# Optimization experiments

Hardware: AMD Instinct MI355X
Metric: run time of the kernel (lower is better)

The kernel has to match this reference:

```python
import jax, jax.numpy as jnp
import numpy as np

B, S, D = 4, 4096, 64

def setup_inputs() -> dict:
    key = jax.random.key(0)
    k1, k2 = jax.random.split(key)
    query = jax.random.normal(k1, (B, S, D), dtype=jnp.float32)
    value = jax.random.normal(k2, (B, S, D), dtype=jnp.float32)
    return {"query": query, "value": value}

def reference(query, value):
    # score = Q @ V^T  -> [B, Sq, Skv]  (note: value acts as both key and value; no 1/sqrt(d) scaling)
    score = jnp.einsum("bqd,bkd->bqk", query, value)
    attn_weights = jax.nn.softmax(score, axis=-1)
    context = jnp.einsum("bqk,bkd->bqd", attn_weights, value)
    return (context, attn_weights)
```

## Files before the change

kernel.cpp:

```cpp
#include <hip/hip_runtime.h>

#define BB 4
#define SS 4096
#define DD 64
#define QB 32
#define TK 64
#define SV 72
#define SP 72

typedef _Float16 h16;
typedef h16 half4_t __attribute__((ext_vector_type(4)));
typedef h16 half8_t __attribute__((ext_vector_type(8)));
typedef float f32x4 __attribute__((ext_vector_type(4)));

struct LdsBufs {
    h16 Vhi[2][TK * SV];
    h16 Vlo[2][TK * SV];
    h16 VTr[2][DD * SV];
    h16 Pl[4][16 * SP];
};

__device__ __forceinline__ void stage(LdsBufs& L, const float* Vb, int it, int t,
                                      bool with_vt) {
    const int ts  = t >> 7;
    const int tt  = t & 127;
    const int c16 = tt & 15;
    const int kr  = tt >> 4;
    const f32x4* Vg = (const f32x4*)(Vb + ((size_t)(it * 2 + ts) * TK + kr * 8) * DD);
    half4_t hh[8];
#pragma unroll
    for (int i = 0; i < 8; ++i) {
        f32x4 v = Vg[i * 16 + c16];
        half4_t hi, lo;
#pragma unroll
        for (int j = 0; j < 4; ++j) {
            float x = v[j];
            h16 h = (h16)x;
            hi[j] = h;
            lo[j] = (h16)(x - (float)h);
        }
        hh[i] = hi;
        *(half4_t*)&L.Vhi[ts][(kr * 8 + i) * SV + c16 * 4] = hi;
        *(half4_t*)&L.Vlo[ts][(kr * 8 + i) * SV + c16 * 4] = lo;
    }
    if (with_vt) {
#pragma unroll
        for (int j = 0; j < 4; ++j) {
            half8_t col;
#pragma unroll
            for (int i = 0; i < 8; ++i) col[i] = hh[i][j];
            *(half8_t*)&L.VTr[ts][(c16 * 4 + j) * SV + kr * 8] = col;
        }
    }
}

__device__ __forceinline__ void scores(const LdsBufs& L, int ts, int qi, int quad,
                                       const half8_t* qhi, const half8_t* qlo,
                                       f32x4* sc) {
#pragma unroll
    for (int mt = 0; mt < 4; ++mt) sc[mt] = (f32x4){0.f, 0.f, 0.f, 0.f};
#pragma unroll
    for (int ks = 0; ks < 2; ++ks) {
#pragma unroll
        for (int mt = 0; mt < 4; ++mt) {
            half8_t ahi = *(const half8_t*)&L.Vhi[ts][(mt * 16 + qi) * SV + ks * 32 + quad * 8];
            half8_t alo = *(const half8_t*)&L.Vlo[ts][(mt * 16 + qi) * SV + ks * 32 + quad * 8];
            sc[mt] = __builtin_amdgcn_mfma_f32_16x16x32_f16(ahi, qhi[ks], sc[mt], 0, 0, 0);
            sc[mt] = __builtin_amdgcn_mfma_f32_16x16x32_f16(ahi, qlo[ks], sc[mt], 0, 0, 0);
            sc[mt] = __builtin_amdgcn_mfma_f32_16x16x32_f16(alo, qhi[ks], sc[mt], 0, 0, 0);
        }
    }
}

__global__ __launch_bounds__(256, 2) void attn_fused(const float* __restrict__ Q,
                                                     const float* __restrict__ V,
                                                     float* __restrict__ ctx,
                                                     float* __restrict__ attn) {
    __shared__ LdsBufs L;
    const int t     = threadIdx.x;
    const int w     = t >> 6;
    const int lane  = t & 63;
    const int qi    = lane & 15;
    const int quad  = lane >> 4;
    const int qgrp  = w & 1;
    const int khalf = w >> 1;
    const int b     = blockIdx.y;
    const int qb    = blockIdx.x * QB + qgrp * 16;

    const float* Vb   = V + (size_t)b * SS * DD;
    const float* Qrow = Q + ((size_t)b * SS + qb + qi) * DD;

    half8_t qhi[2], qlo[2];
#pragma unroll
    for (int ks = 0; ks < 2; ++ks) {
        const float* p = Qrow + ks * 32 + quad * 8;
#pragma unroll
        for (int j = 0; j < 8; ++j) {
            float x = p[j];
            h16 h = (h16)x;
            qhi[ks][j] = h;
            qlo[ks][j] = (h16)(x - (float)h);
        }
    }

    float mrun = -1e30f, lrun = 0.f;
    f32x4 oc[4];
#pragma unroll
    for (int mt = 0; mt < 4; ++mt) oc[mt] = (f32x4){0.f, 0.f, 0.f, 0.f};

    for (int it = 0; it < SS / TK / 2; ++it) {
        __syncthreads();
        stage(L, Vb, it, t, true);
        __syncthreads();

        f32x4 sc[4];
        scores(L, khalf, qi, quad, qhi, qlo, sc);

        float tmax = -1e30f;
#pragma unroll
        for (int mt = 0; mt < 4; ++mt)
#pragma unroll
            for (int r = 0; r < 4; ++r) tmax = fmaxf(tmax, sc[mt][r]);
        tmax = fmaxf(tmax, __shfl_xor(tmax, 16));
        tmax = fmaxf(tmax, __shfl_xor(tmax, 32));
        float mn    = fmaxf(mrun, tmax);
        float alpha = __expf(mrun - mn);
        float psum  = 0.f;
        half4_t pv[4];
#pragma unroll
        for (int mt = 0; mt < 4; ++mt)
#pragma unroll
            for (int r = 0; r < 4; ++r) {
                float p = __expf(sc[mt][r] - mn);
                psum += p;
                pv[mt][r] = (h16)p;
            }
        psum += __shfl_xor(psum, 16);
        psum += __shfl_xor(psum, 32);
        lrun = lrun * alpha + psum;
        mrun = mn;
#pragma unroll
        for (int mt = 0; mt < 4; ++mt) {
            oc[mt] *= alpha;
            *(half4_t*)&L.Pl[w][qi * SP + mt * 16 + quad * 4] = pv[mt];
        }

#pragma unroll
        for (int ks = 0; ks < 2; ++ks) {
            half8_t bp = *(const half8_t*)&L.Pl[w][qi * SP + ks * 32 + quad * 8];
#pragma unroll
            for (int mt = 0; mt < 4; ++mt) {
                half8_t av = *(const half8_t*)&L.VTr[khalf][(mt * 16 + qi) * SV + ks * 32 + quad * 8];
                oc[mt] = __builtin_amdgcn_mfma_f32_16x16x32_f16(av, bp, oc[mt], 0, 0, 0);
            }
        }
    }

    __syncthreads();
    {
        float* buf  = (float*)&L.Vhi[0][0];
        float* mine = buf + (w * 64 + lane) * 18;
        mine[0] = mrun;
        mine[1] = lrun;
#pragma unroll
        for (int mt = 0; mt < 4; ++mt)
#pragma unroll
            for (int r = 0; r < 4; ++r) mine[2 + mt * 4 + r] = oc[mt][r];
        __syncthreads();
        const float* po = buf + ((w ^ 2) * 64 + lane) * 18;
        float m2 = po[0], l2 = po[1];
        float mn = fmaxf(mrun, m2);
        float ea = __expf(mrun - mn), eb = __expf(m2 - mn);
        lrun = lrun * ea + l2 * eb;
#pragma unroll
        for (int mt = 0; mt < 4; ++mt)
#pragma unroll
            for (int r = 0; r < 4; ++r)
                oc[mt][r] = oc[mt][r] * ea + po[2 + mt * 4 + r] * eb;
        mrun = mn;
    }

    const float invl = 1.f / lrun;

    if (khalf == 0) {
        float* crow = ctx + ((size_t)b * SS + qb + qi) * DD;
#pragma unroll
        for (int mt = 0; mt < 4; ++mt) {
            f32x4 cv;
#pragma unroll
            for (int r = 0; r < 4; ++r) cv[r] = oc[mt][r] * invl;
            *(f32x4*)&crow[mt * 16 + quad * 4] = cv;
        }
    }

    float* arow = attn + ((size_t)b * SS + qb + qi) * SS;
    for (int it = 0; it < SS / TK / 2; ++it) {
        __syncthreads();
        stage(L, Vb, it, t, false);
        __syncthreads();

        f32x4 sc[4];
        scores(L, khalf, qi, quad, qhi, qlo, sc);
        const int kt = it * 2 + khalf;
#pragma unroll
        for (int mt = 0; mt < 4; ++mt) {
            f32x4 wv;
#pragma unroll
            for (int r = 0; r < 4; ++r) wv[r] = __expf(sc[mt][r] - mrun) * invl;
            *(f32x4*)&arow[kt * TK + mt * 16 + quad * 4] = wv;
        }
    }
}

extern "C" void kernel_launch(void* const* d_in, const int* in_sizes, int n_in,
                              void* d_out, int out_size, void* d_ws, size_t ws_size,
                              hipStream_t stream) {
    const float* Q = (const float*)d_in[0];
    const float* V = (const float*)d_in[1];
    float* ctx  = (float*)d_out;
    float* attn = (float*)d_out + (size_t)BB * SS * DD;
    attn_fused<<<dim3(SS / QB, BB), 256, 0, stream>>>(Q, V, ctx, attn);
}
```

Before: 385.3 us.

## Precompute split-fp16 V images and stream them via async global-to-LDS loads

```diff
diff --git a/kernel.cpp b/kernel.cpp
--- a/kernel.cpp
+++ b/kernel.cpp
@@ -3,212 +3,280 @@
 #define BB 4
 #define SS 4096
 #define DD 64
-#define QB 32
-#define TK 64
-#define SV 72
-#define SP 72
+#define QB 64
+#define NKI 128
+#define NIT (SS / NKI)
+#define IMGB 49152
 
 typedef _Float16 h16;
-typedef h16 half4_t __attribute__((ext_vector_type(4)));
+typedef h16 half2_t __attribute__((ext_vector_type(2)));
 typedef h16 half8_t __attribute__((ext_vector_type(8)));
 typedef float f32x4 __attribute__((ext_vector_type(4)));
-
-struct LdsBufs {
-    h16 Vhi[2][TK * SV];
-    h16 Vlo[2][TK * SV];
-    h16 VTr[2][DD * SV];
-    h16 Pl[4][16 * SP];
-};
-
-__device__ __forceinline__ void stage(LdsBufs& L, const float* Vb, int it, int t,
-                                      bool with_vt) {
-    const int ts  = t >> 7;
-    const int tt  = t & 127;
-    const int c16 = tt & 15;
-    const int kr  = tt >> 4;
-    const f32x4* Vg = (const f32x4*)(Vb + ((size_t)(it * 2 + ts) * TK + kr * 8) * DD);
-    half4_t hh[8];
-#pragma unroll
-    for (int i = 0; i < 8; ++i) {
-        f32x4 v = Vg[i * 16 + c16];
-        half4_t hi, lo;
+typedef float f32x16 __attribute__((ext_vector_type(16)));
+typedef unsigned u32x4v __attribute__((ext_vector_type(4)));
+
+typedef __attribute__((address_space(3))) uint32_t lds_u32;
+typedef const __attribute__((address_space(1))) uint32_t gl_u32;
+
+#define Z16 ((f32x16){0.f,0.f,0.f,0.f,0.f,0.f,0.f,0.f,0.f,0.f,0.f,0.f,0.f,0.f,0.f,0.f})
+
+template <int NC>
+__device__ __forceinline__ void stage_img(const char* g, char* l, int t) {
+#pragma unroll
+    for (int i = 0; i < NC; ++i) {
+        const int off = (i * 512 + t) * 16;
+        __builtin_amdgcn_global_load_lds((gl_u32*)(g + off), (lds_u32*)(l + off), 16, 0, 0);
+    }
+}
+
+__device__ __forceinline__ unsigned pkh(float a, float b) {
+    half2_t x = {(h16)a, (h16)b};
+    return __builtin_bit_cast(unsigned, x);
+}
+
+__device__ __forceinline__ void xpair(unsigned& wl, unsigned& wh, int h) {
+    unsigned xl = (unsigned)__shfl_xor((int)wl, 32);
+    unsigned xh = (unsigned)__shfl_xor((int)wh, 32);
+    unsigned nl = h ? xh : wl;
+    unsigned nh = h ? wh : xl;
+    wl = nl; wh = nh;
+}
+
+__global__ __launch_bounds__(512) void prep_v(const float* __restrict__ V,
+                                              char* __restrict__ W) {
+    __shared__ h16 VT[64][128];
+    const int t  = threadIdx.x;
+    const int it = blockIdx.x;
+    const int b  = blockIdx.y;
+    const int k  = t >> 2;
+    const int dc = t & 3;
+    char* img = W + ((size_t)b * NIT + it) * IMGB;
+    const float* src = V + ((size_t)b * SS + (size_t)it * NKI + k) * DD + dc * 16;
+#pragma unroll
+    for (int o = 0; o < 2; ++o) {
+        f32x4 a = *(const f32x4*)(src + o * 8);
+        f32x4 c = *(const f32x4*)(src + o * 8 + 4);
+        half8_t hi, lo;
 #pragma unroll
         for (int j = 0; j < 4; ++j) {
-            float x = v[j];
-            h16 h = (h16)x;
-            hi[j] = h;
-            lo[j] = (h16)(x - (float)h);
-        }
-        hh[i] = hi;
-        *(half4_t*)&L.Vhi[ts][(kr * 8 + i) * SV + c16 * 4] = hi;
-        *(half4_t*)&L.Vlo[ts][(kr * 8 + i) * SV + c16 * 4] = lo;
-    }
-    if (with_vt) {
-#pragma unroll
-        for (int j = 0; j < 4; ++j) {
-            half8_t col;
-#pragma unroll
-            for (int i = 0; i < 8; ++i) col[i] = hh[i][j];
-            *(half8_t*)&L.VTr[ts][(c16 * 4 + j) * SV + kr * 8] = col;
-        }
-    }
-}
-
-__device__ __forceinline__ void scores(const LdsBufs& L, int ts, int qi, int quad,
-                                       const half8_t* qhi, const half8_t* qlo,
-                                       f32x4* sc) {
-#pragma unroll
-    for (int mt = 0; mt < 4; ++mt) sc[mt] = (f32x4){0.f, 0.f, 0.f, 0.f};
+            float x = a[j]; h16 hh = (h16)x;
+            hi[j] = hh; lo[j] = (h16)(x - (float)hh);
+            float y = c[j]; h16 gg = (h16)y;
+            hi[j + 4] = gg; lo[j + 4] = (h16)(y - (float)gg);
+        }
+        const int cc = (dc * 2 + o) ^ (k & 7);
+        *(half8_t*)(img + (size_t)k * 128 + cc * 16) = hi;
+        *(half8_t*)(img + 16384 + (size_t)k * 128 + cc * 16) = lo;
+        const int d0 = dc * 16 + o * 8;
+#pragma unroll
+        for (int j = 0; j < 8; ++j) VT[d0 + j][k] = hi[j];
+    }
+    __syncthreads();
+#pragma unroll
+    for (int j = 0; j < 2; ++j) {
+        const int ci = j * 512 + t;
+        const int d  = ci >> 4;
+        const int cc = ci & 15;
+        const int k0 = (cc ^ (d & 7)) * 8;
+        half8_t v = *(const half8_t*)&VT[d][k0];
+        *(half8_t*)(img + 32768 + (size_t)d * 256 + cc * 16) = v;
+    }
+}
+
+__device__ __forceinline__ f32x16 scores32(const char* buf, int kq, int h, int kr, int x7,
+                                           const half8_t* qh, const half8_t* ql) {
+    const char* Vh = buf + (size_t)(kq * 32 + kr) * 128;
+    const char* Vl = Vh + 16384;
+    f32x16 sa = Z16, sb = Z16;
+#pragma unroll
+    for (int s = 0; s < 4; ++s) {
+        const int cc = ((s * 2 + h) ^ x7) << 4;
+        half8_t ah = *(const half8_t*)(Vh + cc);
+        half8_t al = *(const half8_t*)(Vl + cc);
+        if (s & 1) {
+            sb = __builtin_amdgcn_mfma_f32_32x32x16_f16(ah, qh[s], sb, 0, 0, 0);
+            sb = __builtin_amdgcn_mfma_f32_32x32x16_f16(ah, ql[s], sb, 0, 0, 0);
+            sb = __builtin_amdgcn_mfma_f32_32x32x16_f16(al, qh[s], sb, 0, 0, 0);
+        } else {
+            sa = __builtin_amdgcn_mfma_f32_32x32x16_f16(ah, qh[s], sa, 0, 0, 0);
+            sa = __builtin_amdgcn_mfma_f32_32x32x16_f16(ah, ql[s], sa, 0, 0, 0);
+            sa = __builtin_amdgcn_mfma_f32_32x32x16_f16(al, qh[s], sa, 0, 0, 0);
+        }
+    }
+    return sa + sb;
+}
+
+__device__ __forceinline__ void p1_step(const char* buf, int kq, int h, int kr, int x7,
+                                        const half8_t* qh, const half8_t* ql,
+                                        float& mrun, float& lrun, f32x16& oc0, f32x16& oc1) {
+    f32x16 sc = scores32(buf, kq, h, kr, x7, qh, ql);
+
+    float tmax = sc[0];
+#pragma unroll
+    for (int i = 1; i < 16; ++i) tmax = fmaxf(tmax, sc[i]);
+    tmax = fmaxf(tmax, __shfl_xor(tmax, 32));
+    const float mn = fmaxf(mrun, tmax);
+    float p[16], ps = 0.f;
+#pragma unroll
+    for (int i = 0; i < 16; ++i) { p[i] = __expf(sc[i] - mn); ps += p[i]; }
+    ps += __shfl_xor(ps, 32);
+    const bool still = __all(tmax <= mrun);
+    const float alpha = still ? 1.f : __expf(mrun - mn);
+    lrun = lrun * alpha + ps;
+    mrun = mn;
+    if (!still) { oc0 *= alpha; oc1 *= alpha; }
+
+    unsigned w0 = pkh(p[0], p[1]),   w1 = pkh(p[2], p[3]);
+    unsigned w2 = pkh(p[4], p[5]),   w3 = pkh(p[6], p[7]);
+    unsigned w4 = pkh(p[8], p[9]),   w5 = pkh(p[10], p[11]);
+    unsigned w6 = pkh(p[12], p[13]), w7 = pkh(p[14], p[15]);
+    xpair(w0, w2, h); xpair(w1, w3, h); xpair(w4, w6, h); xpair(w5, w7, h);
+    half8_t pb0 = __builtin_bit_cast(half8_t, (u32x4v){w0, w1, w2, w3});
+    half8_t pb1 = __builtin_bit_cast(half8_t, (u32x4v){w4, w5, w6, w7});
+
+    const char* VT = buf + 32768 + (size_t)kr * 256;
 #pragma unroll
     for (int ks = 0; ks < 2; ++ks) {
-#pragma unroll
-        for (int mt = 0; mt < 4; ++mt) {
-            half8_t ahi = *(const half8_t*)&L.Vhi[ts][(mt * 16 + qi) * SV + ks * 32 + quad * 8];
-            half8_t alo = *(const half8_t*)&L.Vlo[ts][(mt * 16 + qi) * SV + ks * 32 + quad * 8];
-            sc[mt] = __builtin_amdgcn_mfma_f32_16x16x32_f16(ahi, qhi[ks], sc[mt], 0, 0, 0);
-            sc[mt] = __builtin_amdgcn_mfma_f32_16x16x32_f16(ahi, qlo[ks], sc[mt], 0, 0, 0);
-            sc[mt] = __builtin_amdgcn_mfma_f32_16x16x32_f16(alo, qhi[ks], sc[mt], 0, 0, 0);
-        }
-    }
-}
-
-__global__ __launch_bounds__(256, 2) void attn_fused(const float* __restrict__ Q,
-                                                     const float* __restrict__ V,
+        const half8_t bp = ks ? pb1 : pb0;
+        const int c0 = ((kq * 4 + ks * 2 + h) ^ x7) << 4;
+        half8_t av0 = *(const half8_t*)(VT + c0);
+        half8_t av1 = *(const half8_t*)(VT + 32 * 256 + c0);
+        oc0 = __builtin_amdgcn_mfma_f32_32x32x16_f16(av0, bp, oc0, 0, 0, 0);
+        oc1 = __builtin_amdgcn_mfma_f32_32x32x16_f16(av1, bp, oc1, 0, 0, 0);
+    }
+}
+
+__device__ __forceinline__ void p2_step(const char* buf, int it, int kq, int h, int kr, int x7,
+                                        const half8_t* qh, const half8_t* ql,
+                                        float moff, float* arow) {
+    f32x16 sc = scores32(buf, kq, h, kr, x7, qh, ql);
+    const int colb = it * NKI + kq * 32 + h * 4;
+#pragma unroll
+    for (int g = 0; g < 4; ++g) {
+        f32x4 wv;
+#pragma unroll
+        for (int m = 0; m < 4; ++m) wv[m] = __expf(sc[g * 4 + m] - moff);
+        __builtin_nontemporal_store(wv, (f32x4*)&arow[colb + g * 8]);
+    }
+}
+
+__global__ __launch_bounds__(512, 2) void attn_fused(const float* __restrict__ Q,
+                                                     const char* __restrict__ W,
                                                      float* __restrict__ ctx,
                                                      float* __restrict__ attn) {
-    __shared__ LdsBufs L;
-    const int t     = threadIdx.x;
-    const int w     = t >> 6;
-    const int lane  = t & 63;
-    const int qi    = lane & 15;
-    const int quad  = lane >> 4;
-    const int qgrp  = w & 1;
-    const int khalf = w >> 1;
-    const int b     = blockIdx.y;
-    const int qb    = blockIdx.x * QB + qgrp * 16;
-
-    const float* Vb   = V + (size_t)b * SS * DD;
-    const float* Qrow = Q + ((size_t)b * SS + qb + qi) * DD;
-
-    half8_t qhi[2], qlo[2];
-#pragma unroll
-    for (int ks = 0; ks < 2; ++ks) {
-        const float* p = Qrow + ks * 32 + quad * 8;
-#pragma unroll
-        for (int j = 0; j < 8; ++j) {
-            float x = p[j];
-            h16 h = (h16)x;
-            qhi[ks][j] = h;
-            qlo[ks][j] = (h16)(x - (float)h);
+    __shared__ __align__(16) char B0[IMGB];
+    __shared__ __align__(16) char B1[IMGB];
+    const int t    = threadIdx.x;
+    const int wid  = t >> 6;
+    const int lane = t & 63;
+    const int kr   = lane & 31;
+    const int h    = lane >> 5;
+    const int x7   = kr & 7;
+    const int qgrp = wid & 1;
+    const int kq   = wid >> 1;
+    const int bid  = blockIdx.x;
+    const int b    = bid & 3;
+    const int qg   = (bid >> 2) * QB + qgrp * 32 + kr;
+
+    const char* Wb    = W + (size_t)b * NIT * IMGB;
+    const float* Qrow = Q + ((size_t)b * SS + qg) * DD;
+
+    half8_t qh[4], ql[4];
+#pragma unroll
+    for (int s = 0; s < 4; ++s) {
+        f32x4 a = *(const f32x4*)(Qrow + s * 16 + h * 8);
+        f32x4 c = *(const f32x4*)(Qrow + s * 16 + h * 8 + 4);
+#pragma unroll
+        for (int j = 0; j < 4; ++j) {
+            float x = a[j]; h16 hh = (h16)x;
+            qh[s][j] = hh; ql[s][j] = (h16)(x - (float)hh);
+            float y = c[j]; h16 gg = (h16)y;
+            qh[s][j + 4] = gg; ql[s][j + 4] = (h16)(y - (float)gg);
         }
     }
 
     float mrun = -1e30f, lrun = 0.f;
-    f32x4 oc[4];
-#pragma unroll
-    for (int mt = 0; mt < 4; ++mt) oc[mt] = (f32x4){0.f, 0.f, 0.f, 0.f};
-
-    for (int it = 0; it < SS / TK / 2; ++it) {
-        __syncthreads();
-        stage(L, Vb, it, t, true);
-        __syncthreads();
-
-        f32x4 sc[4];
-        scores(L, khalf, qi, quad, qhi, qlo, sc);
-
-        float tmax = -1e30f;
-#pragma unroll
-        for (int mt = 0; mt < 4; ++mt)
-#pragma unroll
-            for (int r = 0; r < 4; ++r) tmax = fmaxf(tmax, sc[mt][r]);
-        tmax = fmaxf(tmax, __shfl_xor(tmax, 16));
-        tmax = fmaxf(tmax, __shfl_xor(tmax, 32));
-        float mn    = fmaxf(mrun, tmax);
-        float alpha = __expf(mrun - mn);
-        float psum  = 0.f;
-        half4_t pv[4];
-#pragma unroll
-        for (int mt = 0; mt < 4; ++mt)
-#pragma unroll
-            for (int r = 0; r < 4; ++r) {
-                float p = __expf(sc[mt][r] - mn);
-                psum += p;
-                pv[mt][r] = (h16)p;
-            }
-        psum += __shfl_xor(psum, 16);
-        psum += __shfl_xor(psum, 32);
-        lrun = lrun * alpha + psum;
-        mrun = mn;
-#pragma unroll
-        for (int mt = 0; mt < 4; ++mt) {
-            oc[mt] *= alpha;
-            *(half4_t*)&L.Pl[w][qi * SP + mt * 16 + quad * 4] = pv[mt];
-        }
-
-#pragma unroll
-        for (int ks = 0; ks < 2; ++ks) {
-            half8_t bp = *(const half8_t*)&L.Pl[w][qi * SP + ks * 32 + quad * 8];
-#pragma unroll
-            for (int mt = 0; mt < 4; ++mt) {
-                half8_t av = *(const half8_t*)&L.VTr[khalf][(mt * 16 + qi) * SV + ks * 32 + quad * 8];
-                oc[mt] = __builtin_amdgcn_mfma_f32_16x16x32_f16(av, bp, oc[mt], 0, 0, 0);
-            }
-        }
-    }
-
-    __syncthreads();
+    f32x16 oc0 = Z16, oc1 = Z16;
+
+    stage_img<6>(Wb, B0, t);
+    __syncthreads();
+#pragma unroll 1
+    for (int it = 0; it < NIT; it += 2) {
+        stage_img<6>(Wb + (size_t)(it + 1) * IMGB, B1, t);
+        p1_step(B0, kq, h, kr, x7, qh, ql, mrun, lrun, oc0, oc1);
+        __syncthreads();
+        if (it + 2 < NIT) stage_img<6>(Wb + (size_t)(it + 2) * IMGB, B0, t);
+        p1_step(B1, kq, h, kr, x7, qh, ql, mrun, lrun, oc0, oc1);
+        __syncthreads();
+    }
+
+    float efac[4], mf, lf;
     {
-        float* buf  = (float*)&L.Vhi[0][0];
-        float* mine = buf + (w * 64 + lane) * 18;
-        mine[0] = mrun;
-        mine[1] = lrun;
-#pragma unroll
-        for (int mt = 0; mt < 4; ++mt)
-#pragma unroll
-            for (int r = 0; r < 4; ++r) mine[2 + mt * 4 + r] = oc[mt][r];
-        __syncthreads();
-        const float* po = buf + ((w ^ 2) * 64 + lane) * 18;
-        float m2 = po[0], l2 = po[1];
-        float mn = fmaxf(mrun, m2);
-        float ea = __expf(mrun - mn), eb = __expf(m2 - mn);
-        lrun = lrun * ea + l2 * eb;
-#pragma unroll
-        for (int mt = 0; mt < 4; ++mt)
-#pragma unroll
-            for (int r = 0; r < 4; ++r)
-                oc[mt][r] = oc[mt][r] * ea + po[2 + mt * 4 + r] * eb;
-        mrun = mn;
-    }
+        float* buf  = (float*)B0;
+        float* mine = buf + t * 18;
+        mine[0] = mrun; mine[1] = lrun;
+#pragma unroll
+        for (int i = 0; i < 16; ++i) mine[2 + i] = oc0[i];
+        __syncthreads();
+        mf = -1e30f;
+#pragma unroll
+        for (int k2 = 0; k2 < 4; ++k2)
+            mf = fmaxf(mf, buf[((qgrp + 2 * k2) * 64 + lane) * 18]);
+        lf = 0.f;
+        f32x16 n0 = Z16;
+#pragma unroll
+        for (int k2 = 0; k2 < 4; ++k2) {
+            const float* po = buf + ((qgrp + 2 * k2) * 64 + lane) * 18;
+            float e = __expf(po[0] - mf);
+            efac[k2] = e;
+            lf += po[1] * e;
+#pragma unroll
+            for (int i = 0; i < 16; ++i) n0[i] += po[2 + i] * e;
+        }
+        __syncthreads();
+        float* buf1  = (float*)B1;
+        float* mine1 = buf1 + t * 16;
+#pragma unroll
+        for (int i = 0; i < 16; ++i) mine1[i] = oc1[i];
+        __syncthreads();
+        f32x16 n1 = Z16;
+#pragma unroll
+        for (int k2 = 0; k2 < 4; ++k2) {
+            const float* po = buf1 + ((qgrp + 2 * k2) * 64 + lane) * 16;
+#pragma unroll
+            for (int i = 0; i < 16; ++i) n1[i] += po[i] * efac[k2];
+        }
+        oc0 = n0; oc1 = n1;
+        mrun = mf; lrun = lf;
+    }
+    __syncthreads();
+
+    stage_img<4>(Wb, B0, t);
 
     const float invl = 1.f / lrun;
-
-    if (khalf == 0) {
-        float* crow = ctx + ((size_t)b * SS + qb + qi) * DD;
-#pragma unroll
-        for (int mt = 0; mt < 4; ++mt) {
-            f32x4 cv;
-#pragma unroll
-            for (int r = 0; r < 4; ++r) cv[r] = oc[mt][r] * invl;
-            *(f32x4*)&crow[mt * 16 + quad * 4] = cv;
-        }
-    }
-
-    float* arow = attn + ((size_t)b * SS + qb + qi) * SS;
-    for (int it = 0; it < SS / TK / 2; ++it) {
-        __syncthreads();
-        stage(L, Vb, it, t, false);
-        __syncthreads();
-
-        f32x4 sc[4];
-        scores(L, khalf, qi, quad, qhi, qlo, sc);
-        const int kt = it * 2 + khalf;
-#pragma unroll
-        for (int mt = 0; mt < 4; ++mt) {
-            f32x4 wv;
-#pragma unroll
-            for (int r = 0; r < 4; ++r) wv[r] = __expf(sc[mt][r] - mrun) * invl;
-            *(f32x4*)&arow[kt * TK + mt * 16 + quad * 4] = wv;
-        }
+    if (kq == 0) {
+        float* crow = ctx + ((size_t)b * SS + qg) * DD;
+#pragma unroll
+        for (int g = 0; g < 4; ++g) {
+            f32x4 c0, c1;
+#pragma unroll
+            for (int m = 0; m < 4; ++m) { c0[m] = oc0[g * 4 + m] * invl; c1[m] = oc1[g * 4 + m] * invl; }
+            *(f32x4*)&crow[g * 8 + h * 4] = c0;
+            *(f32x4*)&crow[32 + g * 8 + h * 4] = c1;
+        }
+    }
+    const float moff = mrun + __logf(lrun);
+    float* arow = attn + ((size_t)b * SS + qg) * SS;
+    __syncthreads();
+
+#pragma unroll 1
+    for (int it = 0; it < NIT; it += 2) {
+        stage_img<4>(Wb + (size_t)(it + 1) * IMGB, B1, t);
+        p2_step(B0, it, kq, h, kr, x7, qh, ql, moff, arow);
+        __syncthreads();
+        if (it + 2 < NIT) stage_img<4>(Wb + (size_t)(it + 2) * IMGB, B0, t);
+        p2_step(B1, it + 1, kq, h, kr, x7, qh, ql, moff, arow);
+        __syncthreads();
     }
 }
 
@@ -219,5 +287,7 @@
     const float* V = (const float*)d_in[1];
     float* ctx  = (float*)d_out;
     float* attn = (float*)d_out + (size_t)BB * SS * DD;
-    attn_fused<<<dim3(SS / QB, BB), 256, 0, stream>>>(Q, V, ctx, attn);
-}
+    char* W = (char*)d_ws;
+    prep_v<<<dim3(NIT, BB), 512, 0, stream>>>(V, W);
+    attn_fused<<<dim3(BB * SS / QB), 512, 0, stream>>>(Q, W, ctx, attn);
+}
```

Measured after the change: 449.1 us. 1.17x slower.
